# Performance work log

Measured on AMD Instinct MI355X. Metric: run time of the kernel, lower is better.

Reference implementation:

```python
import jax, jax.numpy as jnp
import numpy as np

B, S, D, H = 2, 512, 1024, 8
DK = D // H
DFF = 4 * D
R = 51
SEP = 64


def setup_inputs() -> dict:
    key = jax.random.key(0)
    ks = jax.random.split(key, 12)
    def w(k, shape, scale=0.02):
        return jax.random.normal(k, shape, jnp.float32) * scale
    return {
        "x": jax.random.normal(ks[0], (B, S, D), jnp.float32),
        "relation": jax.random.randint(ks[1], (B, S, S), 0, R),
        "mask": jnp.ones((B, S, S), jnp.int32),
        "sep_id": SEP,
        "history_reg": jnp.ones((1,), jnp.float32),
        "Wq": w(ks[2], (D, D)), "bq": jnp.zeros((D,), jnp.float32),
        "Wk": w(ks[3], (D, D)), "bk": jnp.zeros((D,), jnp.float32),
        "Wv": w(ks[4], (D, D)), "bv": jnp.zeros((D,), jnp.float32),
        "Wo": w(ks[5], (D, D)), "bo": jnp.zeros((D,), jnp.float32),
        "rel_k_emb": w(ks[6], (R, DK)),
        "rel_v_emb": w(ks[7], (R, DK)),
        "ln1_g": jnp.ones((D,), jnp.float32), "ln1_b": jnp.zeros((D,), jnp.float32),
        "ln2_g": jnp.ones((D,), jnp.float32), "ln2_b": jnp.zeros((D,), jnp.float32),
        "W1": w(ks[8], (D, DFF)), "b1": jnp.zeros((DFF,), jnp.float32),
        "W2": w(ks[9], (DFF, D)), "b2": jnp.zeros((D,), jnp.float32),
    }


def _layer_norm(x, g, b, eps=1e-5):
    m = jnp.mean(x, axis=-1, keepdims=True)
    v = jnp.mean(jnp.square(x - m), axis=-1, keepdims=True)
    return (x - m) * jax.lax.rsqrt(v + eps) * g + b


def _forward(x, relation, mask, sep_id, history_reg, Wq, bq, Wk, bk, Wv, bv, Wo, bo,
             rel_k_emb, rel_v_emb, ln1_g, ln1_b, ln2_g, ln2_b, W1, b1, W2, b2):
    b, s, d = x.shape
    # relation-aware self-attention sublayer (pre-norm)
    h = _layer_norm(x, ln1_g, ln1_b)
    rk = rel_k_emb[relation]  # [B,S,S,DK]
    rv = rel_v_emb[relation]  # [B,S,S,DK]
    def proj(W, bias):
        return (h @ W + bias).reshape(b, s, H, DK).transpose(0, 2, 1, 3)  # [B,H,S,DK]
    q, k, v = proj(Wq, bq), proj(Wk, bk), proj(Wv, bv)
    scores = jnp.einsum("bhid,bhjd->bhij", q, k) + jnp.einsum("bhid,bijd->bhij", q, rk)
    scores = scores / jnp.sqrt(jnp.float32(DK))
    scores = jnp.where(mask[:, None, :, :] == 0, jnp.float32(-1e9), scores)
    attn = jax.nn.softmax(scores, axis=-1)  # [B,H,S,S]
    ctx = jnp.einsum("bhij,bhjd->bhid", attn, v) + jnp.einsum("bhij,bijd->bhid", attn, rv)
    ctx = ctx.transpose(0, 2, 1, 3).reshape(b, s, d)
    attn_out = ctx @ Wo + bo
    # history regularization loss: attention mass on history tokens (positions < sep_id)
    loss = history_reg[0] * jnp.mean(attn[:, :, :, :sep_id])
    x = x + attn_out
    # FFN sublayer (pre-norm)
    h2 = _layer_norm(x, ln2_g, ln2_b)
    ffn = jax.nn.relu(h2 @ W1 + b1) @ W2 + b2
    x = x + ffn
    return x, loss


def reference(x, relation, mask, sep_id, history_reg, Wq, bq, Wk, bk, Wv, bv, Wo, bo,
              rel_k_emb, rel_v_emb, ln1_g, ln1_b, ln2_g, ln2_b, W1, b1, W2, b2):
    return _forward(x, relation, mask, sep_id, history_reg, Wq, bq, Wk, bk, Wv, bv,
                    Wo, bo, rel_k_emb, rel_v_emb, ln1_g, ln1_b, ln2_g, ln2_b,
                    W1, b1, W2, b2)
```

## Files before the change

kernel.cpp:

```cpp
#include <hip/hip_runtime.h>
#include <hip/hip_bf16.h>

#define NB 2
#define NS 512
#define ND 1024
#define NH 8
#define NDK 128
#define NDFF 4096
#define RPAD 64
#define BSROWS 1024
#define NBH 16
#define QT 16
#define SLP 524

typedef __bf16 bf16x8 __attribute__((ext_vector_type(8)));
typedef __bf16 bf16x4 __attribute__((ext_vector_type(4)));
typedef float f32x4 __attribute__((ext_vector_type(4)));

#define BM 64
#define BN 64
#define BK 64

__device__ __forceinline__ void gload16(const void* g, void* l) {
    __builtin_amdgcn_global_load_lds(
        (const __attribute__((address_space(1))) void*)g,
        (__attribute__((address_space(3))) void*)l, 16, 0, 0);
}

__global__ __launch_bounds__(256, 4) void gemm64(
    const __bf16* __restrict__ A, const __bf16* __restrict__ Bt,
    __bf16* __restrict__ vt,
    float* __restrict__ Cf, __bf16* __restrict__ Cb,
    const float* __restrict__ bias,
    int Ksp, int lda, int ldb, int ldc,
    long sA, long sA2, int zdivA,
    long sB, long sB2, int zdivB,
    long sC, int nsplit, long sPart, int flags)
{
    __shared__ __bf16 As0[BM * BK];
    __shared__ __bf16 As1[BM * BK];
    __shared__ __bf16 Bs0[BN * BK];
    __shared__ __bf16 Bs1[BN * BK];

    const unsigned gx = gridDim.x, gy = gridDim.y;
    const unsigned n = gx * gy * gridDim.z;
    const unsigned o = blockIdx.x + gx * (blockIdx.y + gy * blockIdx.z);
    const unsigned q = n >> 3, r = n & 7, xcd = o & 7;
    const unsigned nl = (xcd < r ? xcd * (q + 1) : r * (q + 1) + (xcd - r) * q) + (o >> 3);
    const unsigned bx = nl % gx, tmp = nl / gx;
    const unsigned by = tmp % gy, bz = tmp / gy;

    const int z = bz;
    const int bh = z / nsplit, sp = z - bh * nsplit;
    const long kbase = (long)sp * Ksp;
    A  += (long)(bh / zdivA) * sA + (long)(bh % zdivA) * sA2 + kbase;
    Bt += (long)(bh / zdivB) * sB + (long)(bh % zdivB) * sB2 + kbase;
    const long cbase = (long)bh * sC + (long)sp * sPart;

    const int tM = by * BM, tN = bx * BN;
    const int t = threadIdx.x, lane = t & 63, w = t >> 6;
    const int wr = w >> 1, wc = w & 1;

    const int srow = lane >> 3;
    const int scolE = ((((lane & 7) << 4) ^ (srow << 4)) >> 1);

    const __bf16* gA = A + (long)(tM + srow) * lda + scolE;
    const __bf16* gB = Bt + (long)(tN + srow) * ldb + scolE;

    f32x4 acc[2][2];
#pragma unroll
    for (int m = 0; m < 2; ++m)
#pragma unroll
        for (int nn = 0; nn < 2; ++nn)
#pragma unroll
            for (int j = 0; j < 4; ++j) acc[m][nn][j] = 0.f;

    const int r16 = lane & 15;
    const int kq = (lane >> 4) * 8;
    const int xorE = (r16 & 7) * 8;
    const int nt = Ksp / BK;

    auto STAGE = [&](__bf16* as, __bf16* bs, int k0) {
#pragma unroll
        for (int i = 0; i < 2; ++i) {
            const int rr = (w + i * 4) * 8;
            gload16(gA + (long)rr * lda + k0, (void*)&as[rr * BK]);
            gload16(gB + (long)rr * ldb + k0, (void*)&bs[rr * BK]);
        }
    };
    auto COMPUTE = [&](const __bf16* as, const __bf16* bs) {
        __builtin_amdgcn_s_setprio(1);
#pragma unroll
        for (int ks = 0; ks < 2; ++ks) {
            bf16x8 af[2], bv[2];
#pragma unroll
            for (int m = 0; m < 2; ++m)
                af[m] = *(const bf16x8*)&as[(wr * 32 + m * 16 + r16) * BK + ((ks * 32 + kq) ^ xorE)];
#pragma unroll
            for (int nn = 0; nn < 2; ++nn)
                bv[nn] = *(const bf16x8*)&bs[(wc * 32 + nn * 16 + r16) * BK + ((ks * 32 + kq) ^ xorE)];
#pragma unroll
            for (int m = 0; m < 2; ++m)
#pragma unroll
                for (int nn = 0; nn < 2; ++nn)
                    acc[m][nn] = __builtin_amdgcn_mfma_f32_16x16x32_bf16(af[m], bv[nn], acc[m][nn], 0, 0, 0);
        }
        __builtin_amdgcn_s_setprio(0);
    };

    STAGE(As0, Bs0, 0);
    STAGE(As1, Bs1, BK);
    for (int tt = 0; tt < nt; tt += 2) {
        asm volatile("s_waitcnt vmcnt(4)\n\ts_barrier" ::: "memory");
        COMPUTE(As0, Bs0);
        asm volatile("s_waitcnt lgkmcnt(0)\n\ts_barrier" ::: "memory");
        const bool more = (tt + 2 < nt);
        if (more) {
            STAGE(As0, Bs0, (tt + 2) * BK);
            asm volatile("s_waitcnt vmcnt(4)\n\ts_barrier" ::: "memory");
        } else {
            asm volatile("s_waitcnt vmcnt(0)\n\ts_barrier" ::: "memory");
        }
        COMPUTE(As1, Bs1);
        asm volatile("s_waitcnt lgkmcnt(0)\n\ts_barrier" ::: "memory");
        if (more) STAGE(As1, Bs1, (tt + 3) * BK);
    }

    const bool relu = (flags & 1) != 0;
    const bool vmode = (flags & 8) && (tN >= 2 * ND);
#pragma unroll
    for (int m = 0; m < 2; ++m) {
        const int gr0 = tM + wr * 32 + m * 16 + (lane >> 4) * 4;
#pragma unroll
        for (int nn = 0; nn < 2; ++nn) {
            const int gc = tN + wc * 32 + nn * 16 + (lane & 15);
            const float bb = bias ? bias[gc] : 0.f;
            if (vmode) {
                const int hd = gc - 2 * ND;
                const int b = gr0 >> 9, i = gr0 & 511;
                bf16x4 ov;
#pragma unroll
                for (int j = 0; j < 4; ++j) ov[j] = (__bf16)(acc[m][nn][j] + bb);
                *(bf16x4*)&vt[(((long)b * NH + (hd >> 7)) * NDK + (hd & 127)) * NS + i] = ov;
            } else {
#pragma unroll
                for (int j = 0; j < 4; ++j) {
                    float v = acc[m][nn][j] + bb;
                    if (relu) v = fmaxf(v, 0.f);
                    const long idx = cbase + (long)(gr0 + j) * ldc + gc;
                    if (Cb) Cb[idx] = (__bf16)v;
                    else Cf[idx] = v;
                }
            }
        }
    }
}

__global__ __launch_bounds__(256, 2) void attn_fused(
    const __bf16* __restrict__ qkvb, const __bf16* __restrict__ vt,
    const __bf16* __restrict__ relkT, const __bf16* __restrict__ relvT,
    const int* __restrict__ relation, const int* __restrict__ mask,
    __bf16* __restrict__ ctxm, float* __restrict__ loss_part,
    const int* __restrict__ sep_p)
{
    __shared__ float Sl[QT * SLP];
    __shared__ __bf16 Ks0[64 * NDK];
    __shared__ __bf16 Ks1[64 * NDK];
    __shared__ float qrl[QT][RPAD];
    __shared__ float bins[QT][68];
    __shared__ float redl[4];

    const unsigned o = blockIdx.x + 32u * blockIdx.y;
    const unsigned nl = (o & 7) * 64u + (o >> 3);
    const int qt = nl & 31, bh = nl >> 5;
    const int b = bh >> 3, h = bh & 7;
    const int i0 = qt * QT;

    const int t = threadIdx.x, lane = t & 63, w = t >> 6;
    const int r16 = lane & 15;
    const int kq = (lane >> 4) * 8;
    const int xorE = (r16 & 7) * 8;
    const int sep = *sep_p;

    bf16x8 qf[4];
    {
        const __bf16* qrow = qkvb + ((long)(b * NS + i0 + r16)) * (3 * ND) + h * NDK;
#pragma unroll
        for (int ks = 0; ks < 4; ++ks)
            qf[ks] = *(const bf16x8*)(qrow + ks * 32 + kq);
    }

    {
        f32x4 a;
#pragma unroll
        for (int j = 0; j < 4; ++j) a[j] = 0.f;
#pragma unroll
        for (int ks = 0; ks < 4; ++ks) {
            const bf16x8 bfr = *(const bf16x8*)(relkT + (long)(w * 16 + r16) * NDK + ks * 32 + kq);
            a = __builtin_amdgcn_mfma_f32_16x16x32_bf16(qf[ks], bfr, a, 0, 0, 0);
        }
#pragma unroll
        for (int j = 0; j < 4; ++j)
            qrl[(lane >> 4) * 4 + j][w * 16 + (lane & 15)] = a[j];
    }
    for (int idx = t; idx < QT * 68; idx += 256) ((float*)bins)[idx] = 0.f;

    auto KSTAGE = [&](__bf16* ksb, int kv0) {
#pragma unroll
        for (int ii = 0; ii < 4; ++ii) {
            const int Lc = (w * 4 + ii) * 64 + lane;
            const int j = Lc >> 4, cc = Lc & 15;
            gload16(qkvb + ((long)(b * NS + kv0 + j)) * (3 * ND) + ND + h * NDK + ((cc ^ (j & 7)) << 3),
                    (void*)&ksb[(w * 4 + ii) * 512]);
        }
    };
    auto SCOMP = [&](const __bf16* ksb, int kv0) {
        f32x4 s;
#pragma unroll
        for (int j = 0; j < 4; ++j) s[j] = 0.f;
#pragma unroll
        for (int ks = 0; ks < 4; ++ks) {
            const bf16x8 bfr = *(const bf16x8*)&ksb[(w * 16 + r16) * NDK + ((ks * 32 + kq) ^ xorE)];
            s = __builtin_amdgcn_mfma_f32_16x16x32_bf16(qf[ks], bfr, s, 0, 0, 0);
        }
        const int colb = kv0 + w * 16 + (lane & 15);
#pragma unroll
        for (int j = 0; j < 4; ++j)
            Sl[((lane >> 4) * 4 + j) * SLP + colb] = s[j];
    };

    KSTAGE(Ks0, 0);
    KSTAGE(Ks1, 64);
    for (int tt = 0; tt < 8; tt += 2) {
        asm volatile("s_waitcnt vmcnt(4)\n\ts_barrier" ::: "memory");
        SCOMP(Ks0, tt * 64);
        asm volatile("s_waitcnt lgkmcnt(0)\n\ts_barrier" ::: "memory");
        const bool more = (tt + 2 < 8);
        if (more) {
            KSTAGE(Ks0, (tt + 2) * 64);
            asm volatile("s_waitcnt vmcnt(4)\n\ts_barrier" ::: "memory");
        } else {
            asm volatile("s_waitcnt vmcnt(0)\n\ts_barrier" ::: "memory");
        }
        SCOMP(Ks1, (tt + 1) * 64);
        asm volatile("s_waitcnt lgkmcnt(0)\n\ts_barrier" ::: "memory");
        if (more) KSTAGE(Ks1, (tt + 3) * 64);
    }

    const float sc = 0.088388347648318447f;
    float lsum = 0.f;
#pragma unroll 1
    for (int rr = 0; rr < 4; ++rr) {
        const int row = w * 4 + rr;
        const int* relrow = relation + ((long)(b * NS + i0 + row)) * NS;
        const int* mrow = mask + ((long)(b * NS + i0 + row)) * NS;
        float v[8]; int rl[8];
        float mx = -1e30f;
#pragma unroll
        for (int c = 0; c < 8; ++c) {
            const int j = lane + c * 64;
            const float s = Sl[row * SLP + j];
            rl[c] = relrow[j];
            float vv = (s + qrl[row][rl[c]]) * sc;
            if (mrow[j] == 0) vv = -1e9f;
            v[c] = vv;
            mx = fmaxf(mx, vv);
        }
#pragma unroll
        for (int of = 32; of > 0; of >>= 1) mx = fmaxf(mx, __shfl_xor(mx, of, 64));
        float sm = 0.f;
#pragma unroll
        for (int c = 0; c < 8; ++c) { v[c] = __expf(v[c] - mx); sm += v[c]; }
#pragma unroll
        for (int of = 32; of > 0; of >>= 1) sm += __shfl_xor(sm, of, 64);
        const float inv = 1.f / sm;
#pragma unroll
        for (int c = 0; c < 8; ++c) {
            const float a = v[c] * inv;
            Sl[row * SLP + lane + c * 64] = a;
            atomicAdd(&bins[row][rl[c]], a);
            if (lane + c * 64 < sep) lsum += a;
        }
    }
#pragma unroll
    for (int of = 32; of > 0; of >>= 1) lsum += __shfl_xor(lsum, of, 64);
    if (lane == 0) redl[w] = lsum;
    __syncthreads();
    if (t == 0) loss_part[bh * 32 + qt] = redl[0] + redl[1] + redl[2] + redl[3];

    f32x4 oacc[2];
#pragma unroll
    for (int nn = 0; nn < 2; ++nn)
#pragma unroll
        for (int j = 0; j < 4; ++j) oacc[nn][j] = 0.f;

#pragma unroll
    for (int kc = 0; kc < 16; ++kc) {
        const float4 a0 = *(const float4*)&Sl[r16 * SLP + kc * 32 + kq];
        const float4 a1 = *(const float4*)&Sl[r16 * SLP + kc * 32 + kq + 4];
        bf16x8 af;
        af[0] = (__bf16)a0.x; af[1] = (__bf16)a0.y; af[2] = (__bf16)a0.z; af[3] = (__bf16)a0.w;
        af[4] = (__bf16)a1.x; af[5] = (__bf16)a1.y; af[6] = (__bf16)a1.z; af[7] = (__bf16)a1.w;
#pragma unroll
        for (int nn = 0; nn < 2; ++nn) {
            const bf16x8 bfr = *(const bf16x8*)(vt + ((long)bh * NDK + w * 32 + nn * 16 + r16) * NS + kc * 32 + kq);
            oacc[nn] = __builtin_amdgcn_mfma_f32_16x16x32_bf16(af, bfr, oacc[nn], 0, 0, 0);
        }
    }
#pragma unroll
    for (int kc = 0; kc < 2; ++kc) {
        const float4 b0 = *(const float4*)&bins[r16][kc * 32 + kq];
        const float4 b1 = *(const float4*)&bins[r16][kc * 32 + kq + 4];
        bf16x8 af;
        af[0] = (__bf16)b0.x; af[1] = (__bf16)b0.y; af[2] = (__bf16)b0.z; af[3] = (__bf16)b0.w;
        af[4] = (__bf16)b1.x; af[5] = (__bf16)b1.y; af[6] = (__bf16)b1.z; af[7] = (__bf16)b1.w;
#pragma unroll
        for (int nn = 0; nn < 2; ++nn) {
            const bf16x8 bfr = *(const bf16x8*)(relvT + (long)(w * 32 + nn * 16 + r16) * RPAD + kc * 32 + kq);
            oacc[nn] = __builtin_amdgcn_mfma_f32_16x16x32_bf16(af, bfr, oacc[nn], 0, 0, 0);
        }
    }
#pragma unroll
    for (int nn = 0; nn < 2; ++nn)
#pragma unroll
        for (int j = 0; j < 4; ++j) {
            const int row = (lane >> 4) * 4 + j;
            ctxm[((long)(b * NS + i0 + row)) * ND + h * NDK + w * 32 + nn * 16 + (lane & 15)] =
                (__bf16)oacc[nn][j];
        }
}

__global__ void prep_weights(
    const float* __restrict__ Wq, const float* __restrict__ Wk,
    const float* __restrict__ Wv, const float* __restrict__ Wo,
    const float* __restrict__ W1, const float* __restrict__ W2,
    const float* __restrict__ relv,
    const float* __restrict__ bq, const float* __restrict__ bk,
    const float* __restrict__ bv, const float* __restrict__ relk,
    const float* __restrict__ x, const float* __restrict__ ln1g,
    const float* __restrict__ ln1b,
    __bf16* __restrict__ WqkvT, __bf16* __restrict__ WoT,
    __bf16* __restrict__ W1T, __bf16* __restrict__ W2T,
    __bf16* __restrict__ relvT, float* __restrict__ biasqkv,
    __bf16* __restrict__ relkT, __bf16* __restrict__ h1, int R)
{
    const int tile = blockIdx.x;
    const int t = threadIdx.y * 32 + threadIdx.x;

    if (tile >= 12372) {
        const long row = tile - 12372;
        const float* xr = x + row * ND;
        float4 v = reinterpret_cast<const float4*>(xr)[t];
        float s = v.x + v.y + v.z + v.w;
        float s2 = v.x * v.x + v.y * v.y + v.z * v.z + v.w * v.w;
#pragma unroll
        for (int o = 32; o > 0; o >>= 1) {
            s += __shfl_xor(s, o, 64);
            s2 += __shfl_xor(s2, o, 64);
        }
        __shared__ float red[8];
        const int lane = t & 63, wv = t >> 6;
        if (lane == 0) { red[wv] = s; red[4 + wv] = s2; }
        __syncthreads();
        s = red[0] + red[1] + red[2] + red[3];
        s2 = red[4] + red[5] + red[6] + red[7];
        const float mean = s * (1.f / ND);
        const float var = s2 * (1.f / ND) - mean * mean;
        const float rs = rsqrtf(var + 1e-5f);
        const float xv[4] = {v.x, v.y, v.z, v.w};
        bf16x4 o;
#pragma unroll
        for (int j = 0; j < 4; ++j) {
            const int c = t * 4 + j;
            o[j] = (__bf16)((xv[j] - mean) * rs * ln1g[c] + ln1b[c]);
        }
        *(bf16x4*)&h1[row * ND + t * 4] = o;
        return;
    }
    if (tile >= 12296) {
        const int ft = (tile - 12296) * 256 + t;
        if (ft < ND) biasqkv[ft] = bq[ft];
        else if (ft < 2 * ND) biasqkv[ft] = bk[ft - ND];
        else if (ft < 3 * ND) biasqkv[ft] = bv[ft - 2 * ND];
        else {
            const int idx = ft - 3 * ND;
            if (idx < 128 * NDK) {
                const int r = idx / NDK;
                relkT[idx] = (r < R) ? (__bf16)relk[idx] : (__bf16)0.f;
            }
        }
        return;
    }
    const float* src; __bf16* dst;
    int rows_in, cols_in, ldo, kx, ny;
    if (tile < 4096) {
        const int m = tile >> 10, r = tile & 1023;
        kx = r & 31; ny = r >> 5;
        rows_in = 1024; cols_in = 1024; ldo = 1024;
        src = m == 0 ? Wq : m == 1 ? Wk : m == 2 ? Wv : Wo;
        dst = m == 3 ? WoT : WqkvT + (size_t)m * 1024 * 1024;
    } else if (tile < 8192) {
        const int r = tile - 4096;
        kx = r & 31; ny = r >> 5;
        rows_in = 1024; cols_in = 4096; ldo = 1024; src = W1; dst = W1T;
    } else if (tile < 12288) {
        const int r = tile - 8192;
        kx = r & 127; ny = r >> 7;
        rows_in = 4096; cols_in = 1024; ldo = 4096; src = W2; dst = W2T;
    } else {
        const int r = tile - 12288;
        kx = r & 1; ny = r >> 1;
        rows_in = R; cols_in = 128; ldo = 64; src = relv; dst = relvT;
    }

    __shared__ float tl[32][33];
    const int k0 = kx * 32, n0 = ny * 32;
    const int tx = threadIdx.x, ty = threadIdx.y;
#pragma unroll
    for (int dy = 0; dy < 32; dy += 8) {
        const int k = k0 + ty + dy, nn = n0 + tx;
        tl[ty + dy][tx] = (k < rows_in && nn < cols_in) ? src[(long)k * cols_in + nn] : 0.f;
    }
    __syncthreads();
#pragma unroll
    for (int dy = 0; dy < 32; dy += 8) {
        const int nn = n0 + ty + dy, k = k0 + tx;
        if (nn < cols_in && k < ldo) dst[(long)nn * ldo + k] = (__bf16)tl[tx][ty + dy];
    }
}

__global__ __launch_bounds__(256) void wo_reduce_ln(
    const float* __restrict__ P, const float* __restrict__ x,
    const float* __restrict__ bo, const float* __restrict__ g,
    const float* __restrict__ bb, float* __restrict__ out,
    __bf16* __restrict__ h2)
{
    const int row = blockIdx.x;
    const int t = threadIdx.x;
    const long i4 = (long)row * 256 + t;
    const long sP = (long)BSROWS * ND / 4;
    const float4* P4 = (const float4*)P;
    float4 s = P4[i4];
    const float4 t1 = P4[i4 + sP];
    s.x += t1.x; s.y += t1.y; s.z += t1.z; s.w += t1.w;
    const int col = t * 4;
    const float4 xv = ((const float4*)x)[i4];
    const float4 bv = *(const float4*)&bo[col];
    float4 o;
    o.x = s.x + xv.x + bv.x; o.y = s.y + xv.y + bv.y;
    o.z = s.z + xv.z + bv.z; o.w = s.w + xv.w + bv.w;
    ((float4*)out)[i4] = o;

    float sum = o.x + o.y + o.z + o.w;
    float sum2 = o.x * o.x + o.y * o.y + o.z * o.z + o.w * o.w;
#pragma unroll
    for (int of = 32; of > 0; of >>= 1) {
        sum += __shfl_xor(sum, of, 64);
        sum2 += __shfl_xor(sum2, of, 64);
    }
    __shared__ float red[8];
    const int lane = t & 63, wv = t >> 6;
    if (lane == 0) { red[wv] = sum; red[4 + wv] = sum2; }
    __syncthreads();
    sum = red[0] + red[1] + red[2] + red[3];
    sum2 = red[4] + red[5] + red[6] + red[7];
    const float mean = sum * (1.f / ND);
    const float var = sum2 * (1.f / ND) - mean * mean;
    const float rs = rsqrtf(var + 1e-5f);
    const float ov[4] = {o.x, o.y, o.z, o.w};
    bf16x4 hb;
#pragma unroll
    for (int j = 0; j < 4; ++j)
        hb[j] = (__bf16)((ov[j] - mean) * rs * g[col + j] + bb[col + j]);
    *(bf16x4*)&h2[(long)row * ND + col] = hb;
}

__global__ __launch_bounds__(256) void ffn2_reduce(
    const float* __restrict__ P, const float* __restrict__ b2, float* __restrict__ out,
    const float* __restrict__ loss_part, const float* __restrict__ hist,
    const int* __restrict__ sep_p, float* __restrict__ out_loss)
{
    const int i4 = blockIdx.x * 256 + threadIdx.x;
    const long sP = (long)BSROWS * ND / 4;
    const float4* P4 = (const float4*)P;
    float4 s = P4[i4];
    const float4 t1 = P4[i4 + sP];
    s.x += t1.x; s.y += t1.y; s.z += t1.z; s.w += t1.w;
    const int col = (i4 * 4) & (ND - 1);
    const float4 bv = *(const float4*)&b2[col];
    float4 o = ((float4*)out)[i4];
    o.x += s.x + bv.x; o.y += s.y + bv.y;
    o.z += s.z + bv.z; o.w += s.w + bv.w;
    ((float4*)out)[i4] = o;

    if (blockIdx.x == 0) {
        const int t = threadIdx.x;
        float ls = 0.f;
        if (t < 128) {
            const float4 v = ((const float4*)loss_part)[t];
            ls = v.x + v.y + v.z + v.w;
        }
#pragma unroll
        for (int of = 32; of > 0; of >>= 1) ls += __shfl_xor(ls, of, 64);
        __shared__ float red[4];
        if ((t & 63) == 0) red[t >> 6] = ls;
        __syncthreads();
        if (t == 0) {
            const int sep = *sep_p;
            const float total = red[0] + red[1] + red[2] + red[3];
            const float denom = (float)NB * NH * NS * (float)(sep > 0 ? sep : 1);
            out_loss[0] = (sep > 0) ? hist[0] * total / denom : 0.f;
        }
    }
}

extern "C" void kernel_launch(void* const* d_in, const int* in_sizes, int n_in,
                              void* d_out, int out_size, void* d_ws, size_t ws_size,
                              hipStream_t stream)
{
    const float* x      = (const float*)d_in[0];
    const int* relation = (const int*)d_in[1];
    const int* mask     = (const int*)d_in[2];
    const int* sep_p    = (const int*)d_in[3];
    const float* hist   = (const float*)d_in[4];
    const float* Wq = (const float*)d_in[5],  *bq = (const float*)d_in[6];
    const float* Wk = (const float*)d_in[7],  *bk = (const float*)d_in[8];
    const float* Wv = (const float*)d_in[9],  *bv = (const float*)d_in[10];
    const float* Wo = (const float*)d_in[11], *bo = (const float*)d_in[12];
    const float* relk = (const float*)d_in[13];
    const float* relv = (const float*)d_in[14];
    const float* ln1g = (const float*)d_in[15], *ln1b = (const float*)d_in[16];
    const float* ln2g = (const float*)d_in[17], *ln2b = (const float*)d_in[18];
    const float* W1 = (const float*)d_in[19], *b1 = (const float*)d_in[20];
    const float* W2 = (const float*)d_in[21], *b2 = (const float*)d_in[22];
    const int R = in_sizes[13] / NDK;

    float* out = (float*)d_out;
    float* out_loss = out + (long)BSROWS * ND;

    char* p = (char*)d_ws;
    auto alloc = [&](size_t bytes) -> void* {
        void* r = (void*)p;
        p += (bytes + 255) & ~(size_t)255;
        return r;
    };
    __bf16* WqkvT   = (__bf16*)alloc((size_t)3 * ND * ND * 2);
    __bf16* WoT     = (__bf16*)alloc((size_t)ND * ND * 2);
    __bf16* W1T     = (__bf16*)alloc((size_t)NDFF * ND * 2);
    __bf16* W2T     = (__bf16*)alloc((size_t)ND * NDFF * 2);
    __bf16* relkT   = (__bf16*)alloc((size_t)128 * NDK * 2);
    __bf16* relvT   = (__bf16*)alloc((size_t)NDK * RPAD * 2);
    float*  biasqkv = (float*)alloc((size_t)3 * ND * 4);
    __bf16* h1      = (__bf16*)alloc((size_t)BSROWS * ND * 2);
    __bf16* qkvb    = (__bf16*)alloc((size_t)BSROWS * 3 * ND * 2);
    __bf16* vt      = (__bf16*)alloc((size_t)NBH * NDK * NS * 2);
    __bf16* ctxm    = (__bf16*)alloc((size_t)BSROWS * ND * 2);
    __bf16* h2      = (__bf16*)alloc((size_t)BSROWS * ND * 2);
    __bf16* F1      = (__bf16*)alloc((size_t)BSROWS * NDFF * 2);
    float*  loss_part = (float*)alloc((size_t)512 * 4);
    float*  arena   = (float*)alloc((size_t)16 * 1024 * 1024);
    float* woPart   = arena;
    float* f2Part   = arena + (size_t)2 * 1024 * 1024;

    const dim3 tb(32, 8);
    prep_weights<<<13396, tb, 0, stream>>>(Wq, Wk, Wv, Wo, W1, W2, relv,
                                           bq, bk, bv, relk, x, ln1g, ln1b,
                                           WqkvT, WoT, W1T, W2T, relvT,
                                           biasqkv, relkT, h1, R);

    gemm64<<<dim3(48, 16, 1), 256, 0, stream>>>(
        h1, WqkvT, vt, nullptr, qkvb, biasqkv,
        ND, ND, ND, 3 * ND,
        0, 0, 1, 0, 0, 1, 0, 1, 0, 8);

    attn_fused<<<dim3(32, 16), 256, 0, stream>>>(
        qkvb, vt, relkT, relvT, relation, mask, ctxm, loss_part, sep_p);

    gemm64<<<dim3(16, 16, 2), 256, 0, stream>>>(
        ctxm, WoT, nullptr, woPart, nullptr, nullptr,
        512, ND, ND, ND,
        0, 0, 1, 0, 0, 1,
        0, 2, (long)BSROWS * ND, 0);

    wo_reduce_ln<<<BSROWS, 256, 0, stream>>>(woPart, x, bo, ln2g, ln2b, out, h2);

    gemm64<<<dim3(64, 16, 1), 256, 0, stream>>>(
        h2, W1T, nullptr, nullptr, F1, b1,
        ND, ND, ND, NDFF,
        0, 0, 1, 0, 0, 1, 0, 1, 0, 1);

    gemm64<<<dim3(16, 16, 2), 256, 0, stream>>>(
        F1, W2T, nullptr, f2Part, nullptr, nullptr,
        2048, NDFF, NDFF, ND,
        0, 0, 1, 0, 0, 1,
        0, 2, (long)BSROWS * ND, 0);

    ffn2_reduce<<<1024, 256, 0, stream>>>(f2Part, b2, out,
                                          loss_part, hist, sep_p, out_loss);
}
```

Before: 131.4 us.

## Stage V through double-buffered LDS and prefetch relation/mask in attention

The attention kernel now keeps the score tile in LDS as bf16 instead of fp32, which halves its footprint and drops the fp32-to-bf16 conversion before the PV MFMAs. Relation and mask rows are loaded into registers as int4 vectors at kernel start, so their latency overlaps the QK^T phase. Each lane's softmax columns become contiguous (lane*8+q) rather than strided by 64. The PV product now streams V tiles through the existing double-buffered K LDS buffers using async global-to-LDS loads with swizzling, raised wave priority and explicit waitcnt barriers. The cost is more registers for the prefetched rows, which could limit occupancy, and slightly lower precision in the stored scores.

```diff
diff --git a/kernel.cpp b/kernel.cpp
--- a/kernel.cpp
+++ b/kernel.cpp
@@ -11,7 +11,7 @@
 #define BSROWS 1024
 #define NBH 16
 #define QT 16
-#define SLP 524
+#define SLB 536
 
 typedef __bf16 bf16x8 __attribute__((ext_vector_type(8)));
 typedef __bf16 bf16x4 __attribute__((ext_vector_type(4)));
@@ -163,7 +163,7 @@
     __bf16* __restrict__ ctxm, float* __restrict__ loss_part,
     const int* __restrict__ sep_p)
 {
-    __shared__ float Sl[QT * SLP];
+    __shared__ __bf16 Sl[QT * SLB];
     __shared__ __bf16 Ks0[64 * NDK];
     __shared__ __bf16 Ks1[64 * NDK];
     __shared__ float qrl[QT][RPAD];
@@ -190,6 +190,16 @@
             qf[ks] = *(const bf16x8*)(qrow + ks * 32 + kq);
     }
 
+    int4 ra[4][2], ma[4][2];
+#pragma unroll
+    for (int rr = 0; rr < 4; ++rr) {
+        const long rg = (long)(b * NS + i0 + w * 4 + rr) * NS;
+        ra[rr][0] = ((const int4*)(relation + rg))[lane * 2];
+        ra[rr][1] = ((const int4*)(relation + rg))[lane * 2 + 1];
+        ma[rr][0] = ((const int4*)(mask + rg))[lane * 2];
+        ma[rr][1] = ((const int4*)(mask + rg))[lane * 2 + 1];
+    }
+
     {
         f32x4 a;
 #pragma unroll
@@ -226,7 +236,7 @@
         const int colb = kv0 + w * 16 + (lane & 15);
 #pragma unroll
         for (int j = 0; j < 4; ++j)
-            Sl[((lane >> 4) * 4 + j) * SLP + colb] = s[j];
+            Sl[((lane >> 4) * 4 + j) * SLB + colb] = (__bf16)s[j];
     };
 
     KSTAGE(Ks0, 0);
@@ -247,45 +257,60 @@
         if (more) KSTAGE(Ks1, (tt + 3) * 64);
     }
 
+    auto VSTAGE = [&](__bf16* vs, int kv0) {
+#pragma unroll
+        for (int ii = 0; ii < 4; ++ii) {
+            const int d = w * 32 + ii * 8 + (lane >> 3);
+            const int cc = lane & 7;
+            gload16(vt + ((long)bh * NDK + d) * NS + kv0 + ((cc ^ (d & 7)) << 3),
+                    (void*)&vs[(w * 32 + ii * 8) * 64]);
+        }
+    };
+    VSTAGE(Ks0, 0);
+    VSTAGE(Ks1, 64);
+
     const float sc = 0.088388347648318447f;
     float lsum = 0.f;
-#pragma unroll 1
+#pragma unroll
     for (int rr = 0; rr < 4; ++rr) {
         const int row = w * 4 + rr;
-        const int* relrow = relation + ((long)(b * NS + i0 + row)) * NS;
-        const int* mrow = mask + ((long)(b * NS + i0 + row)) * NS;
-        float v[8]; int rl[8];
+        const bf16x8 sv = *(const bf16x8*)&Sl[row * SLB + lane * 8];
+        int rl[8], mm[8];
+        rl[0] = ra[rr][0].x; rl[1] = ra[rr][0].y; rl[2] = ra[rr][0].z; rl[3] = ra[rr][0].w;
+        rl[4] = ra[rr][1].x; rl[5] = ra[rr][1].y; rl[6] = ra[rr][1].z; rl[7] = ra[rr][1].w;
+        mm[0] = ma[rr][0].x; mm[1] = ma[rr][0].y; mm[2] = ma[rr][0].z; mm[3] = ma[rr][0].w;
+        mm[4] = ma[rr][1].x; mm[5] = ma[rr][1].y; mm[6] = ma[rr][1].z; mm[7] = ma[rr][1].w;
+        float v[8];
         float mx = -1e30f;
 #pragma unroll
-        for (int c = 0; c < 8; ++c) {
-            const int j = lane + c * 64;
-            const float s = Sl[row * SLP + j];
-            rl[c] = relrow[j];
-            float vv = (s + qrl[row][rl[c]]) * sc;
-            if (mrow[j] == 0) vv = -1e9f;
-            v[c] = vv;
+        for (int q = 0; q < 8; ++q) {
+            float vv = ((float)sv[q] + qrl[row][rl[q]]) * sc;
+            if (mm[q] == 0) vv = -1e9f;
+            v[q] = vv;
             mx = fmaxf(mx, vv);
         }
 #pragma unroll
         for (int of = 32; of > 0; of >>= 1) mx = fmaxf(mx, __shfl_xor(mx, of, 64));
         float sm = 0.f;
 #pragma unroll
-        for (int c = 0; c < 8; ++c) { v[c] = __expf(v[c] - mx); sm += v[c]; }
+        for (int q = 0; q < 8; ++q) { v[q] = __expf(v[q] - mx); sm += v[q]; }
 #pragma unroll
         for (int of = 32; of > 0; of >>= 1) sm += __shfl_xor(sm, of, 64);
         const float inv = 1.f / sm;
-#pragma unroll
-        for (int c = 0; c < 8; ++c) {
-            const float a = v[c] * inv;
-            Sl[row * SLP + lane + c * 64] = a;
-            atomicAdd(&bins[row][rl[c]], a);
-            if (lane + c * 64 < sep) lsum += a;
-        }
+        bf16x8 av;
+#pragma unroll
+        for (int q = 0; q < 8; ++q) {
+            const float a = v[q] * inv;
+            av[q] = (__bf16)a;
+            atomicAdd(&bins[row][rl[q]], a);
+            if (lane * 8 + q < sep) lsum += a;
+        }
+        *(bf16x8*)&Sl[row * SLB + lane * 8] = av;
     }
 #pragma unroll
     for (int of = 32; of > 0; of >>= 1) lsum += __shfl_xor(lsum, of, 64);
     if (lane == 0) redl[w] = lsum;
-    __syncthreads();
+    asm volatile("s_waitcnt lgkmcnt(0)\n\ts_barrier" ::: "memory");
     if (t == 0) loss_part[bh * 32 + qt] = redl[0] + redl[1] + redl[2] + redl[3];
 
     f32x4 oacc[2];
@@ -294,19 +319,36 @@
 #pragma unroll
         for (int j = 0; j < 4; ++j) oacc[nn][j] = 0.f;
 
-#pragma unroll
-    for (int kc = 0; kc < 16; ++kc) {
-        const float4 a0 = *(const float4*)&Sl[r16 * SLP + kc * 32 + kq];
-        const float4 a1 = *(const float4*)&Sl[r16 * SLP + kc * 32 + kq + 4];
-        bf16x8 af;
-        af[0] = (__bf16)a0.x; af[1] = (__bf16)a0.y; af[2] = (__bf16)a0.z; af[3] = (__bf16)a0.w;
-        af[4] = (__bf16)a1.x; af[5] = (__bf16)a1.y; af[6] = (__bf16)a1.z; af[7] = (__bf16)a1.w;
-#pragma unroll
-        for (int nn = 0; nn < 2; ++nn) {
-            const bf16x8 bfr = *(const bf16x8*)(vt + ((long)bh * NDK + w * 32 + nn * 16 + r16) * NS + kc * 32 + kq);
-            oacc[nn] = __builtin_amdgcn_mfma_f32_16x16x32_bf16(af, bfr, oacc[nn], 0, 0, 0);
-        }
-    }
+    auto PVCOMP = [&](const __bf16* vs, int kv0) {
+        __builtin_amdgcn_s_setprio(1);
+#pragma unroll
+        for (int ks = 0; ks < 2; ++ks) {
+            const bf16x8 af = *(const bf16x8*)&Sl[r16 * SLB + kv0 + ks * 32 + kq];
+#pragma unroll
+            for (int nn = 0; nn < 2; ++nn) {
+                const bf16x8 bv = *(const bf16x8*)&vs[(w * 32 + nn * 16 + r16) * 64 + ((ks * 32 + kq) ^ xorE)];
+                oacc[nn] = __builtin_amdgcn_mfma_f32_16x16x32_bf16(af, bv, oacc[nn], 0, 0, 0);
+            }
+        }
+        __builtin_amdgcn_s_setprio(0);
+    };
+
+    for (int tt = 0; tt < 8; tt += 2) {
+        asm volatile("s_waitcnt vmcnt(4)\n\ts_barrier" ::: "memory");
+        PVCOMP(Ks0, tt * 64);
+        asm volatile("s_waitcnt lgkmcnt(0)\n\ts_barrier" ::: "memory");
+        const bool more = (tt + 2 < 8);
+        if (more) {
+            VSTAGE(Ks0, (tt + 2) * 64);
+            asm volatile("s_waitcnt vmcnt(4)\n\ts_barrier" ::: "memory");
+        } else {
+            asm volatile("s_waitcnt vmcnt(0)\n\ts_barrier" ::: "memory");
+        }
+        PVCOMP(Ks1, (tt + 1) * 64);
+        asm volatile("s_waitcnt lgkmcnt(0)\n\ts_barrier" ::: "memory");
+        if (more) VSTAGE(Ks1, (tt + 3) * 64);
+    }
+
 #pragma unroll
     for (int kc = 0; kc < 2; ++kc) {
         const float4 b0 = *(const float4*)&bins[r16][kc * 32 + kq];
```

Result: no change. 131.3 us (-0.1%).
